# Kernel optimization log

Hardware: AMD Instinct MI355X
Metric: run time of the kernel (lower is better)

## Reference

```python
import jax, jax.numpy as jnp
import numpy as np

MAX_K_QK = 64
MAX_K_V = 64
MAX_K_KNOW = 128


def threshold_gate(scores, tau, max_k):
    # scores: [B,S,N], tau: [B,S,1]
    raw = scores - tau
    gate = jnp.where(raw > 0, raw, 1e-08 * jnp.exp(raw))
    exp_gate = jnp.exp(gate) - 1.0
    k = min(max_k, scores.shape[-1])
    topk_vals, _ = jax.lax.top_k(exp_gate, k)
    threshold = topk_vals[:, :, -1:]
    exp_gate = jnp.where(exp_gate >= threshold, exp_gate, 0.0)
    gate_sum = exp_gate.sum(axis=-1, keepdims=True) + 1e-08
    gate_strength = jnp.tanh(exp_gate.max(axis=-1, keepdims=True))
    return exp_gate / gate_sum * gate_strength


def setup_inputs() -> dict:
    key = jax.random.key(0)
    ks = jax.random.split(key, 8)
    B, S, D = 2, 2048, 1024
    N_QK, N_V, N_KNOW = 4096, 4096, 8192
    scale = 0.02  # keep scores in a sane range for exp()
    return {
        "x": jax.random.normal(ks[0], (B, S, D), jnp.float32),
        "qk_emb": jax.random.normal(ks[1], (N_QK, D), jnp.float32) * scale,
        "v_emb": jax.random.normal(ks[2], (N_V, D), jnp.float32) * scale,
        "know_emb": jax.random.normal(ks[3], (N_KNOW, D), jnp.float32) * scale,
        "w_attn": jax.random.normal(ks[4], (D, 3), jnp.float32) * scale,
        "b_attn": jnp.zeros((3,), jnp.float32),
        "w_know": jax.random.normal(ks[5], (D, 1), jnp.float32) * scale,
        "b_know": jnp.zeros((1,), jnp.float32),
    }


def reference(x, qk_emb, v_emb, know_emb, w_attn, b_attn, w_know, b_know):
    # deterministic=True -> router dropout is identity
    # attention gates
    scores_qk = jnp.einsum("bsd,nd->bsn", x, qk_emb)
    scores_v = jnp.einsum("bsd,nd->bsn", x, v_emb)
    tau_all = x @ w_attn + b_attn  # [B,S,3]
    g_Q = threshold_gate(scores_qk, tau_all[:, :, 0:1], MAX_K_QK)
    g_K = threshold_gate(scores_qk, tau_all[:, :, 1:2], MAX_K_QK)
    g_V = threshold_gate(scores_v, tau_all[:, :, 2:3], MAX_K_V)
    t_qk = 1.0 / qk_emb.shape[0]
    t_v = 1.0 / v_emb.shape[0]
    aux_attn = (
        ((g_Q.mean(axis=(0, 1)) - t_qk) ** 2).sum() * g_Q.shape[-1]
        + ((g_K.mean(axis=(0, 1)) - t_qk) ** 2).sum() * g_K.shape[-1]
        + ((g_V.mean(axis=(0, 1)) - t_v) ** 2).sum() * g_V.shape[-1]
    )
    # knowledge gates
    scores_know = jnp.einsum("bsd,nd->bsn", x, know_emb)
    tau_know = x @ w_know + b_know  # [B,S,1]
    g_know = threshold_gate(scores_know, tau_know, MAX_K_KNOW)
    t_know = 1.0 / know_emb.shape[0]
    aux_know = ((g_know.mean(axis=(0, 1)) - t_know) ** 2).sum() * g_know.shape[-1]
    return (g_Q, g_K, g_V, aux_attn, g_know, aux_know)
```

## Files before the change

### kernel.cpp

```cpp
#include <hip/hip_runtime.h>
#include <hip/hip_bf16.h>


#define M_ROWS 4096
#define DIM    1024
#define N_QK   4096
#define N_KNOW 8192

typedef unsigned short ushortT;
typedef __attribute__((ext_vector_type(8)))  short short8;
typedef __attribute__((ext_vector_type(16))) float f32x16;

__global__ __launch_bounds__(256) void tau_kernel(
    const float* __restrict__ x, const float* __restrict__ w_attn,
    const float* __restrict__ b_attn, const float* __restrict__ w_know,
    const float* __restrict__ b_know, float* __restrict__ tau4, int D)
{
    __shared__ float s_f[4][4];
    const int row = blockIdx.x;
    const int tid = threadIdx.x;
    const float* xr = x + (size_t)row * D;
    float p0 = 0.f, p1 = 0.f, p2 = 0.f, p3 = 0.f;
    for (int d = tid; d < D; d += 256) {
        float xv = xr[d];
        p0 += xv * w_attn[d * 3 + 0];
        p1 += xv * w_attn[d * 3 + 1];
        p2 += xv * w_attn[d * 3 + 2];
        p3 += xv * w_know[d];
    }
#pragma unroll
    for (int o = 32; o > 0; o >>= 1) {
        p0 += __shfl_down(p0, o, 64);
        p1 += __shfl_down(p1, o, 64);
        p2 += __shfl_down(p2, o, 64);
        p3 += __shfl_down(p3, o, 64);
    }
    const int lane = tid & 63, wv = tid >> 6;
    if (lane == 0) { s_f[wv][0] = p0; s_f[wv][1] = p1; s_f[wv][2] = p2; s_f[wv][3] = p3; }
    __syncthreads();
    if (tid < 4) {
        float v = s_f[0][tid] + s_f[1][tid] + s_f[2][tid] + s_f[3][tid];
        v += (tid < 3) ? b_attn[tid] : b_know[0];
        tau4[(size_t)row * 4 + tid] = v;
    }
}

__device__ __forceinline__ void split4(const float4 v, uint2& H, uint2& L) {
    float vv[4] = {v.x, v.y, v.z, v.w};
    unsigned h[4], l[4];
#pragma unroll
    for (int i = 0; i < 4; i++) {
        __hip_bfloat16 hb = __float2bfloat16(vv[i]);
        float r = vv[i] - __bfloat162float(hb);
        __hip_bfloat16 lb = __float2bfloat16(r);
        h[i] = *(ushortT*)&hb;
        l[i] = *(ushortT*)&lb;
    }
    H.x = h[0] | (h[1] << 16); H.y = h[2] | (h[3] << 16);
    L.x = l[0] | (l[1] << 16); L.y = l[2] | (l[3] << 16);
}

__global__ __launch_bounds__(256) void convertA(
    const float* __restrict__ src, ushortT* __restrict__ dst, int nElem4)
{
    int g = blockIdx.x * 256 + threadIdx.x;
    if (g >= nElem4) return;
    int row = g >> 8;
    int c4  = g & 255;
    int chunk = c4 >> 3, pos = c4 & 7;
    const float4 v = *(const float4*)(src + (size_t)row * DIM + c4 * 4);
    uint2 H, L;
    split4(v, H, L);
    ushortT* base = dst + (size_t)row * 2048 + chunk * 64;
    *(uint2*)(base + pos * 4)      = H;
    *(uint2*)(base + 32 + pos * 4) = L;
}

__global__ __launch_bounds__(256) void gemm_fused2(
    const ushortT* __restrict__ Aext, const float* __restrict__ qk_emb,
    const float* __restrict__ v_emb, const float* __restrict__ know_emb,
    float* __restrict__ gQ, float* __restrict__ gV, float* __restrict__ gKn,
    long long rowOff)
{
    __shared__ ushortT AHL[128 * 64];
    __shared__ ushortT BHL[128 * 64];
    const int tid = threadIdx.x;
    const int wave = tid >> 6, lane = tid & 63;
    const int l32 = lane & 31, h = lane >> 5;
    const int rx7 = l32 & 7;
    const int wm = (wave >> 1) * 64, wn = (wave & 1) * 64;
    const long long m0 = (long long)blockIdx.y * 128;
    const int nblk = blockIdx.x;

    const float* Bsrc; float* C; long long ldc; long long n0;
    if (nblk < 32)      { Bsrc = qk_emb;   C = gQ;  ldc = N_QK;   n0 = (long long)nblk * 128; }
    else if (nblk < 64) { Bsrc = v_emb;    C = gV;  ldc = N_QK;   n0 = (long long)(nblk - 32) * 128; }
    else                { Bsrc = know_emb; C = gKn; ldc = N_KNOW; n0 = (long long)(nblk - 64) * 128; }

    const ushortT* gAp[4]; ushortT* lAp[4];
    const float*   gBp[4]; int offH[4], offL[4];
#pragma unroll
    for (int it = 0; it < 4; ++it) {
        int f = it * 256 + tid;
        int r = f >> 3, sp = f & 7;
        int sg = sp ^ (r & 7);
        gAp[it] = Aext + (m0 + r) * 2048 + sg * 8;
        lAp[it] = AHL + f * 8;
        int c4 = f & 7;
        int s = c4 >> 1, hf = c4 & 1;
        offH[it] = r * 128 + ((s ^ (r & 7)) * 16) + hf * 8;
        offL[it] = r * 128 + (((4 | s) ^ (r & 7)) * 16) + hf * 8;
        gBp[it] = Bsrc + (n0 + r) * DIM + c4 * 4;
    }
    const char* pA[2]; const char* pB[2];
#pragma unroll
    for (int t = 0; t < 2; ++t) {
        pA[t] = (const char*)AHL + (wm + t * 32 + l32) * 128;
        pB[t] = (const char*)BHL + (wn + t * 32 + l32) * 128;
    }

    f32x16 acc[2][2] = {};
    float4 bufB[4];
#pragma unroll
    for (int it = 0; it < 4; ++it) bufB[it] = *(const float4*)(gBp[it]);

    for (int c = 0; c < 32; ++c) {
#pragma unroll
        for (int it = 0; it < 4; ++it) {
            __builtin_amdgcn_global_load_lds(
                (const __attribute__((address_space(1))) unsigned*)(const void*)(gAp[it] + c * 64),
                (__attribute__((address_space(3))) unsigned*)(void*)lAp[it], 16, 0, 0);
            uint2 H, L;
            split4(bufB[it], H, L);
            *(uint2*)((char*)BHL + offH[it]) = H;
            *(uint2*)((char*)BHL + offL[it]) = L;
        }
        __syncthreads();
        if (c + 1 < 32) {
#pragma unroll
            for (int it = 0; it < 4; ++it)
                bufB[it] = *(const float4*)(gBp[it] + (c + 1) * 32);
        }
#pragma unroll
        for (int kb = 0; kb < 2; ++kb) {
            const int so = ((kb * 2 + h) ^ rx7) * 16;
            short8 aH[2], aL[2], bH[2], bL[2];
#pragma unroll
            for (int t = 0; t < 2; ++t) {
                aH[t] = *(const short8*)(pA[t] + so);
                aL[t] = *(const short8*)(pA[t] + (so ^ 64));
                bH[t] = *(const short8*)(pB[t] + so);
                bL[t] = *(const short8*)(pB[t] + (so ^ 64));
            }
#pragma unroll
            for (int i = 0; i < 2; ++i)
#pragma unroll
                for (int j = 0; j < 2; ++j) {
                    acc[i][j] = __builtin_amdgcn_mfma_f32_32x32x16_bf16(aH[i], bH[j], acc[i][j], 0, 0, 0);
                    acc[i][j] = __builtin_amdgcn_mfma_f32_32x32x16_bf16(aH[i], bL[j], acc[i][j], 0, 0, 0);
                    acc[i][j] = __builtin_amdgcn_mfma_f32_32x32x16_bf16(aL[i], bH[j], acc[i][j], 0, 0, 0);
                    acc[i][j] = __builtin_amdgcn_mfma_f32_32x32x16_bf16(aL[i], bL[j], acc[i][j], 0, 0, 0);
                }
        }
        __syncthreads();
    }
#pragma unroll
    for (int ti = 0; ti < 2; ++ti)
#pragma unroll
        for (int tj = 0; tj < 2; ++tj) {
            long long col = n0 + wn + tj * 32 + l32;
            long long rb  = rowOff + m0 + wm + ti * 32 + 4 * h;
#pragma unroll
            for (int reg = 0; reg < 16; ++reg) {
                long long row = rb + (reg & 3) + 8 * (reg >> 2);
                C[row * ldc + col] = acc[ti][tj][reg];
            }
        }
}

__device__ __forceinline__ unsigned floatToKey(float f) {
    unsigned b = __float_as_uint(f);
    return (b & 0x80000000u) ? ~b : (b | 0x80000000u);
}
__device__ __forceinline__ float keyToFloat(unsigned key) {
    unsigned b = (key & 0x80000000u) ? (key & 0x7FFFFFFFu) : ~key;
    return __uint_as_float(b);
}
__device__ __forceinline__ float egate(float raw) {
    float g = raw > 0.f ? raw : 1e-8f * __expf(raw);
    return expf(g) - 1.f;
}

template <int NV, bool VLOAD, bool VSTORE>
__device__ __forceinline__ void gate_body(
    const float* __restrict__ srow, float tA, float tB, bool hasB, int ksel,
    float* __restrict__ orowA, float* __restrict__ orowB,
    float* __restrict__ colA, float* __restrict__ colB,
    int* s_cnt, unsigned* s_u, float* s_f)
{
    const int tid = threadIdx.x, lane = tid & 63, wv = tid >> 6;

    unsigned keys[NV * 4];
    unsigned kmax = 0u;
#pragma unroll
    for (int i = 0; i < NV; i++) {
        float v0, v1, v2, v3;
        if (VLOAD) {
            float4 v = *(const float4*)(srow + (size_t)(i * 256 + tid) * 4);
            v0 = v.x; v1 = v.y; v2 = v.z; v3 = v.w;
        } else {
            v0 = srow[(i * 4 + 0) * 256 + tid];
            v1 = srow[(i * 4 + 1) * 256 + tid];
            v2 = srow[(i * 4 + 2) * 256 + tid];
            v3 = srow[(i * 4 + 3) * 256 + tid];
        }
        unsigned a = floatToKey(v0), b = floatToKey(v1);
        unsigned c = floatToKey(v2), d = floatToKey(v3);
        keys[i * 4 + 0] = a; keys[i * 4 + 1] = b;
        keys[i * 4 + 2] = c; keys[i * 4 + 3] = d;
        unsigned m1 = a > b ? a : b, m2 = c > d ? c : d;
        m1 = m1 > m2 ? m1 : m2;
        kmax = kmax > m1 ? kmax : m1;
    }
#pragma unroll
    for (int o = 32; o > 0; o >>= 1) {
        unsigned x = __shfl_down(kmax, o, 64);
        kmax = kmax > x ? kmax : x;
    }
    if (lane == 0) s_u[wv] = kmax;
    __syncthreads();
    { unsigned a = s_u[0], b = s_u[1], c = s_u[2], d = s_u[3];
      unsigned m1 = a > b ? a : b, m2 = c > d ? c : d; kmax = m1 > m2 ? m1 : m2; }

    unsigned lo = 0u, hi = kmax, vk;
    int pp = 0;
    for (;;) {
        if (lo >= hi) { vk = lo; break; }
        unsigned mid = lo + ((hi - lo + 1u) >> 1);
        int c = 0;
#pragma unroll
        for (int i = 0; i < NV * 4; i++) c += (keys[i] >= mid) ? 1 : 0;
#pragma unroll
        for (int o = 32; o > 0; o >>= 1) c += __shfl_down(c, o, 64);
        if (lane == 0) s_cnt[pp * 4 + wv] = c;
        __syncthreads();
        int total = s_cnt[pp * 4 + 0] + s_cnt[pp * 4 + 1]
                  + s_cnt[pp * 4 + 2] + s_cnt[pp * 4 + 3];
        pp ^= 1;
        if (total == ksel) { vk = mid; break; }
        if (total > ksel) lo = mid; else hi = mid - 1u;
    }

    float sA = 0.f, sB = 0.f;
#pragma unroll
    for (int i = 0; i < NV * 4; i++) {
        if (keys[i] >= vk) {
            float s = keyToFloat(keys[i]);
            sA += egate(s - tA);
            if (hasB) sB += egate(s - tB);
        }
    }
#pragma unroll
    for (int o = 32; o > 0; o >>= 1) {
        sA += __shfl_down(sA, o, 64);
        sB += __shfl_down(sB, o, 64);
    }
    if (lane == 0) { s_f[wv] = sA; s_f[4 + wv] = sB; }
    __syncthreads();
    sA = s_f[0] + s_f[1] + s_f[2] + s_f[3];
    sB = s_f[4] + s_f[5] + s_f[6] + s_f[7];

    const float smax = keyToFloat(kmax);
    const float scaleA = tanhf(egate(smax - tA)) / (sA + 1e-8f);
    const float scaleB = hasB ? tanhf(egate(smax - tB)) / (sB + 1e-8f) : 0.f;

#pragma unroll
    for (int i = 0; i < NV; i++) {
        float ga[4], gb[4];
        int eidx[4];
#pragma unroll
        for (int j = 0; j < 4; j++) {
            int ii = i * 4 + j;
            int idx = VLOAD ? (i * 1024 + tid * 4 + j) : (ii * 256 + tid);
            eidx[j] = idx;
            unsigned key = keys[ii];
            float vA = 0.f, vB = 0.f;
            if (key >= vk) {
                float s = keyToFloat(key);
                vA = egate(s - tA) * scaleA;
                atomicAdd(&colA[idx], vA);
                if (hasB) { vB = egate(s - tB) * scaleB; atomicAdd(&colB[idx], vB); }
            }
            ga[j] = vA; gb[j] = vB;
        }
        if (VSTORE) {
            *(float4*)(orowA + (size_t)eidx[0]) = make_float4(ga[0], ga[1], ga[2], ga[3]);
            if (hasB) *(float4*)(orowB + (size_t)eidx[0]) = make_float4(gb[0], gb[1], gb[2], gb[3]);
        } else {
#pragma unroll
            for (int j = 0; j < 4; j++) {
                orowA[eidx[j]] = ga[j];
                if (hasB) orowB[eidx[j]] = gb[j];
            }
        }
    }
}

__global__ __launch_bounds__(256) void gate_all(
    const float* __restrict__ tau4,
    float* __restrict__ gQ, float* __restrict__ gK,
    float* __restrict__ gV, float* __restrict__ gKn,
    float* __restrict__ colsums)
{
    __shared__ int s_cnt[8];
    __shared__ unsigned s_u[4];
    __shared__ float s_f[8];
    const int bid = blockIdx.x;
    if (bid < 4096) {
        const int row = bid;
        const float t = tau4[(size_t)row * 4 + 3];
        gate_body<8, false, false>(
            gKn + (size_t)row * N_KNOW, t, 0.f, false, 128,
            gKn + (size_t)row * N_KNOW, nullptr,
            colsums + 3 * N_QK, nullptr, s_cnt, s_u, s_f);
    } else if (bid < 8192) {
        const int row = bid - 4096;
        const float tA = tau4[(size_t)row * 4 + 0];
        const float tB = tau4[(size_t)row * 4 + 1];
        gate_body<4, true, true>(
            gQ + (size_t)row * N_QK, tA, tB, true, 64,
            gQ + (size_t)row * N_QK, gK + (size_t)row * N_QK,
            colsums, colsums + N_QK, s_cnt, s_u, s_f);
    } else {
        const int row = bid - 8192;
        const float t = tau4[(size_t)row * 4 + 2];
        gate_body<4, true, true>(
            gV + (size_t)row * N_QK, t, 0.f, false, 64,
            gV + (size_t)row * N_QK, nullptr,
            colsums + 2 * N_QK, nullptr, s_cnt, s_u, s_f);
    }
}

__global__ __launch_bounds__(256) void aux_kernel(
    const float* __restrict__ colsum,
    float* __restrict__ auxAttn, float* __restrict__ auxKnow)
{
    __shared__ float s_a[4];
    __shared__ float s_b[4];
    const int tid = threadIdx.x;
    const int lane = tid & 63, wv = tid >> 6;
    const float invM = 1.f / 4096.f;

    float sa = 0.f;
    const float tqk = 1.f / 4096.f;
    for (int i = tid; i < 3 * N_QK; i += 256) {
        float m = colsum[i] * invM - tqk;
        sa += m * m;
    }
    float sk = 0.f;
    const float tkn = 1.f / 8192.f;
    for (int i = tid; i < N_KNOW; i += 256) {
        float m = colsum[3 * N_QK + i] * invM - tkn;
        sk += m * m;
    }
#pragma unroll
    for (int o = 32; o > 0; o >>= 1) {
        sa += __shfl_down(sa, o, 64);
        sk += __shfl_down(sk, o, 64);
    }
    if (lane == 0) { s_a[wv] = sa; s_b[wv] = sk; }
    __syncthreads();
    if (tid == 0) {
        auxAttn[0] = (s_a[0] + s_a[1] + s_a[2] + s_a[3]) * 4096.f;
        auxKnow[0] = (s_b[0] + s_b[1] + s_b[2] + s_b[3]) * 8192.f;
    }
}

extern "C" void kernel_launch(void* const* d_in, const int* in_sizes, int n_in,
                              void* d_out, int out_size, void* d_ws, size_t ws_size,
                              hipStream_t stream)
{
    const float* x        = (const float*)d_in[0];
    const float* qk_emb   = (const float*)d_in[1];
    const float* v_emb    = (const float*)d_in[2];
    const float* know_emb = (const float*)d_in[3];
    const float* w_attn   = (const float*)d_in[4];
    const float* b_attn   = (const float*)d_in[5];
    const float* w_know   = (const float*)d_in[6];
    const float* b_know   = (const float*)d_in[7];
    float* out = (float*)d_out;

    const long long M = M_ROWS;

    float* gQ   = out;
    float* gK   = gQ + (size_t)M * N_QK;
    float* gV   = gK + (size_t)M * N_QK;
    float* auxA = gV + (size_t)M * N_QK;
    float* gKn  = auxA + 1;
    float* auxK = gKn + (size_t)M * N_KNOW;

    const long long nColsum = 3 * N_QK + N_KNOW;
    const long long tail_bytes = (M * 4 + nColsum) * 4;
    long long tailStart = ((long long)ws_size - tail_bytes) & ~255LL;
    float* tau4 = (float*)((char*)d_ws + tailStart);
    float* colsums = tau4 + (size_t)M * 4;

    const long long rowB = 4096;
    long long ra = (tailStart / rowB / 128) * 128;
    if (ra > M) ra = M;
    if (ra < 128) ra = 128;
    ushortT* A_ext = (ushortT*)d_ws;

    hipMemsetAsync(colsums, 0, nColsum * sizeof(float), stream);
    tau_kernel<<<(int)M, 256, 0, stream>>>(x, w_attn, b_attn, w_know, b_know, tau4, DIM);

    for (long long a0 = 0; a0 < M; a0 += ra) {
        long long ac = (M - a0 < ra) ? (M - a0) : ra;
        int nel4 = (int)(ac * 256);
        convertA<<<(nel4 + 255) / 256, 256, 0, stream>>>(x + a0 * DIM, A_ext, nel4);
        gemm_fused2<<<dim3(128, (unsigned)(ac / 128)), 256, 0, stream>>>(
            A_ext, qk_emb, v_emb, know_emb, gQ, gV, gKn, a0);
    }

    gate_all<<<12288, 256, 0, stream>>>(tau4, gQ, gK, gV, gKn, colsums);

    aux_kernel<<<1, 256, 0, stream>>>(colsums, auxA, auxK);
}
```

Before: 1.076 ms.

## Pre-split B operands to bf16 hi/lo and double-buffer GEMM via direct LDS loads

Adds a GEMM variant that reads pre-converted bf16 hi/lo embedding matrices from workspace instead of converting fp32 B tiles inside the kernel. It double-buffers A and B tiles in LDS using global_load_lds so loads overlap MFMA compute. The B conversion runs in column chunks sized to the available workspace, and the old path remains as a fallback when workspace is too small. This costs extra conversion passes and workspace traffic for B, and uses twice the LDS, which may lower occupancy.

```diff
diff --git a/kernel.cpp b/kernel.cpp
--- a/kernel.cpp
+++ b/kernel.cpp
@@ -74,6 +74,105 @@
     ushortT* base = dst + (size_t)row * 2048 + chunk * 64;
     *(uint2*)(base + pos * 4)      = H;
     *(uint2*)(base + 32 + pos * 4) = L;
+}
+
+__global__ __launch_bounds__(256) void gemm_fused3(
+    const ushortT* __restrict__ Aext, const ushortT* __restrict__ Bext,
+    float* __restrict__ gQ, float* __restrict__ gV, float* __restrict__ gKn,
+    int nb0)
+{
+    __shared__ ushortT AHL[2][128 * 64];
+    __shared__ ushortT BHL[2][128 * 64];
+    const int tid = threadIdx.x;
+    const int wave = tid >> 6, lane = tid & 63;
+    const int l32 = lane & 31, h = lane >> 5;
+    const int rx7 = l32 & 7;
+    const int wm = (wave >> 1) * 64, wn = (wave & 1) * 64;
+    const long long m0 = (long long)blockIdx.y * 128;
+    const int nblk = nb0 + blockIdx.x;
+
+    float* C; long long ldc; long long n0;
+    if (nblk < 32)      { C = gQ;  ldc = N_QK;   n0 = (long long)nblk * 128; }
+    else if (nblk < 64) { C = gV;  ldc = N_QK;   n0 = (long long)(nblk - 32) * 128; }
+    else                { C = gKn; ldc = N_KNOW; n0 = (long long)(nblk - 64) * 128; }
+
+    const ushortT* gAp[4]; const ushortT* gBp[4]; int lOff[4];
+#pragma unroll
+    for (int it = 0; it < 4; ++it) {
+        int f = it * 256 + tid;
+        int r = f >> 3, sp = f & 7;
+        int sg = sp ^ (r & 7);
+        gAp[it] = Aext + (m0 + r) * 2048 + sg * 8;
+        gBp[it] = Bext + ((long long)blockIdx.x * 128 + r) * 2048 + sg * 8;
+        lOff[it] = f * 8;
+    }
+
+    f32x16 acc[2][2] = {};
+
+#define STAGE(buf, c) do {                                                         \
+    _Pragma("unroll")                                                              \
+    for (int it = 0; it < 4; ++it) {                                               \
+        __builtin_amdgcn_global_load_lds(                                          \
+            (const __attribute__((address_space(1))) unsigned*)(const void*)(gAp[it] + (c) * 64), \
+            (__attribute__((address_space(3))) unsigned*)(void*)(&AHL[buf][0] + lOff[it]), 16, 0, 0); \
+        __builtin_amdgcn_global_load_lds(                                          \
+            (const __attribute__((address_space(1))) unsigned*)(const void*)(gBp[it] + (c) * 64), \
+            (__attribute__((address_space(3))) unsigned*)(void*)(&BHL[buf][0] + lOff[it]), 16, 0, 0); \
+    }                                                                              \
+} while (0)
+
+#define COMPUTE(buf) do {                                                          \
+    _Pragma("unroll")                                                              \
+    for (int kb = 0; kb < 2; ++kb) {                                               \
+        const int so = ((kb * 2 + h) ^ rx7) * 16;                                  \
+        short8 aH[2], aL[2], bH[2], bL[2];                                         \
+        _Pragma("unroll")                                                          \
+        for (int t = 0; t < 2; ++t) {                                              \
+            const char* pa = (const char*)(&AHL[buf][0]) + (wm + t * 32 + l32) * 128; \
+            const char* pb = (const char*)(&BHL[buf][0]) + (wn + t * 32 + l32) * 128; \
+            aH[t] = *(const short8*)(pa + so);                                     \
+            aL[t] = *(const short8*)(pa + (so ^ 64));                              \
+            bH[t] = *(const short8*)(pb + so);                                     \
+            bL[t] = *(const short8*)(pb + (so ^ 64));                              \
+        }                                                                          \
+        _Pragma("unroll")                                                          \
+        for (int i = 0; i < 2; ++i)                                                \
+            _Pragma("unroll")                                                      \
+            for (int j = 0; j < 2; ++j) {                                          \
+                acc[i][j] = __builtin_amdgcn_mfma_f32_32x32x16_bf16(aH[i], bH[j], acc[i][j], 0, 0, 0); \
+                acc[i][j] = __builtin_amdgcn_mfma_f32_32x32x16_bf16(aH[i], bL[j], acc[i][j], 0, 0, 0); \
+                acc[i][j] = __builtin_amdgcn_mfma_f32_32x32x16_bf16(aL[i], bH[j], acc[i][j], 0, 0, 0); \
+                acc[i][j] = __builtin_amdgcn_mfma_f32_32x32x16_bf16(aL[i], bL[j], acc[i][j], 0, 0, 0); \
+            }                                                                      \
+    }                                                                              \
+} while (0)
+
+    STAGE(0, 0);
+    __syncthreads();
+
+    for (int c = 0; c < 32; c += 2) {
+        STAGE(1, c + 1);
+        COMPUTE(0);
+        __syncthreads();
+        if (c + 2 < 32) STAGE(0, c + 2);
+        COMPUTE(1);
+        __syncthreads();
+    }
+#undef STAGE
+#undef COMPUTE
+
+#pragma unroll
+    for (int ti = 0; ti < 2; ++ti)
+#pragma unroll
+        for (int tj = 0; tj < 2; ++tj) {
+            long long col = n0 + wn + tj * 32 + l32;
+            long long rb  = m0 + wm + ti * 32 + 4 * h;
+#pragma unroll
+            for (int reg = 0; reg < 16; ++reg) {
+                long long row = rb + (reg & 3) + 8 * (reg >> 2);
+                C[row * ldc + col] = acc[ti][tj][reg];
+            }
+        }
 }
 
 __global__ __launch_bounds__(256) void gemm_fused2(
@@ -376,6 +475,24 @@
     }
 }
 
+static void convert_b_range(const float* qk, const float* v, const float* kn,
+                            ushortT* Bext, long long rowLo, long long rowHi,
+                            hipStream_t stream)
+{
+    struct Seg { const float* p; long long lo, hi; };
+    Seg seg[3] = { {qk, 0, 4096}, {v, 4096, 8192}, {kn, 8192, 16384} };
+    for (int i = 0; i < 3; ++i) {
+        long long lo = rowLo > seg[i].lo ? rowLo : seg[i].lo;
+        long long hi = rowHi < seg[i].hi ? rowHi : seg[i].hi;
+        if (lo < hi) {
+            int nel4 = (int)((hi - lo) * 256);
+            convertA<<<(nel4 + 255) / 256, 256, 0, stream>>>(
+                seg[i].p + (size_t)(lo - seg[i].lo) * DIM,
+                Bext + (size_t)(lo - rowLo) * 2048, nel4);
+        }
+    }
+}
+
 extern "C" void kernel_launch(void* const* d_in, const int* in_sizes, int n_in,
                               void* d_out, int out_size, void* d_ws, size_t ws_size,
                               hipStream_t stream)
@@ -406,20 +523,38 @@
     float* colsums = tau4 + (size_t)M * 4;
 
     const long long rowB = 4096;
-    long long ra = (tailStart / rowB / 128) * 128;
-    if (ra > M) ra = M;
-    if (ra < 128) ra = 128;
-    ushortT* A_ext = (ushortT*)d_ws;
+    const long long aBytes = M * rowB;
 
     hipMemsetAsync(colsums, 0, nColsum * sizeof(float), stream);
     tau_kernel<<<(int)M, 256, 0, stream>>>(x, w_attn, b_attn, w_know, b_know, tau4, DIM);
 
-    for (long long a0 = 0; a0 < M; a0 += ra) {
-        long long ac = (M - a0 < ra) ? (M - a0) : ra;
-        int nel4 = (int)(ac * 256);
-        convertA<<<(nel4 + 255) / 256, 256, 0, stream>>>(x + a0 * DIM, A_ext, nel4);
-        gemm_fused2<<<dim3(128, (unsigned)(ac / 128)), 256, 0, stream>>>(
-            A_ext, qk_emb, v_emb, know_emb, gQ, gV, gKn, a0);
+    long long availB = tailStart - aBytes;
+    long long nbc = availB > 0 ? availB / (128 * rowB) : 0;
+    if (nbc > 128) nbc = 128;
+
+    if (nbc >= 32) {
+        ushortT* A_ext = (ushortT*)d_ws;
+        ushortT* B_ext = (ushortT*)((char*)d_ws + aBytes);
+        convertA<<<(int)(M * 256 / 256), 256, 0, stream>>>(x, A_ext, (int)(M * 256));
+        for (long long nb0 = 0; nb0 < 128; nb0 += nbc) {
+            long long nn = (128 - nb0 < nbc) ? (128 - nb0) : nbc;
+            convert_b_range(qk_emb, v_emb, know_emb, B_ext,
+                            nb0 * 128, (nb0 + nn) * 128, stream);
+            gemm_fused3<<<dim3((unsigned)nn, 32), 256, 0, stream>>>(
+                A_ext, B_ext, gQ, gV, gKn, (int)nb0);
+        }
+    } else {
+        long long ra = (tailStart / rowB / 128) * 128;
+        if (ra > M) ra = M;
+        if (ra < 128) ra = 128;
+        ushortT* A_ext = (ushortT*)d_ws;
+        for (long long a0 = 0; a0 < M; a0 += ra) {
+            long long ac = (M - a0 < ra) ? (M - a0) : ra;
+            int nel4 = (int)(ac * 256);
+            convertA<<<(nel4 + 255) / 256, 256, 0, stream>>>(x + a0 * DIM, A_ext, nel4);
+            gemm_fused2<<<dim3(128, (unsigned)(ac / 128)), 256, 0, stream>>>(
+                A_ext, qk_emb, v_emb, know_emb, gQ, gV, gKn, a0);
+        }
     }
 
     gate_all<<<12288, 256, 0, stream>>>(tau4, gQ, gK, gV, gKn, colsums);
```

Result: faster. 1.053 ms (-2.1%).
